# Performance work log

Hardware: AMD Instinct MI355X
Metric: run time of the kernel (lower is better)

Reference implementation:

```python
import jax, jax.numpy as jnp
import numpy as np

EPS = 1e-5
G, N, H, P, K = 8, 128, 64, 64, 4  # n_groups, d_state, n_heads, head_dim, conv kernel
R = H // G  # heads per group


def _rmsnorm(x, w, eps=EPS):
    return x * jax.lax.rsqrt(jnp.mean(x * x, axis=-1, keepdims=True) + eps) * w


def setup_inputs() -> dict:
    key = jax.random.key(0)
    ks = jax.random.split(key, 8)
    B, L, Dm = 2, 1024, 2048
    d_inner = 2 * Dm                      # 4096
    conv_dim = d_inner + 2 * G * N        # 6144
    proj_dim = 2 * d_inner + 2 * G * N + H  # 10304
    return {
        "hidden_states": jax.random.normal(ks[0], (B, L, Dm), jnp.float32),
        "residual": jax.random.normal(ks[1], (B, L, Dm), jnp.float32),
        "norm_w": jnp.ones((Dm,), jnp.float32),
        "in_proj_w": jax.random.normal(ks[2], (proj_dim, Dm), jnp.float32) * 0.02,
        "conv_w": jax.random.normal(ks[3], (conv_dim, K), jnp.float32) * 0.1,
        "conv_b": jnp.zeros((conv_dim,), jnp.float32),
        "A_log": jnp.log(jnp.arange(1, H + 1, dtype=jnp.float32)),
        "D_param": jnp.ones((H,), jnp.float32),
        "dt_bias": jax.random.uniform(ks[4], (H,), jnp.float32, -4.0, -1.0),
        "gate_norm_w": jnp.ones((d_inner,), jnp.float32),
        "out_proj_w": jax.random.normal(ks[5], (Dm, d_inner), jnp.float32) * 0.02,
    }


def reference(hidden_states, residual, norm_w, in_proj_w, conv_w, conv_b,
              A_log, D_param, dt_bias, gate_norm_w, out_proj_w):
    B, L, Dm = hidden_states.shape
    d_inner = 2 * Dm
    conv_dim = d_inner + 2 * G * N

    # fused residual-add RMSNorm (residual is not None branch)
    h = hidden_states + residual
    new_residual = h
    x = _rmsnorm(h, norm_w)

    # in_proj -> [z | xBC | dt]
    proj = jnp.einsum('bld,ed->ble', x, in_proj_w)
    z = proj[..., :d_inner]
    xBC = proj[..., d_inner:d_inner + conv_dim]
    dt = proj[..., d_inner + conv_dim:]            # [B, L, H]

    # causal depthwise conv1d over xBC, then SiLU
    lhs = jnp.transpose(xBC, (0, 2, 1))            # [B, C, L]
    rhs = conv_w[:, None, :]                       # [C, 1, K]
    conv = jax.lax.conv_general_dilated(
        lhs, rhs, window_strides=(1,), padding=[(K - 1, 0)],
        feature_group_count=conv_dim)
    xBC = jax.nn.silu(jnp.transpose(conv, (0, 2, 1)) + conv_b)

    xs = xBC[..., :d_inner].reshape(B, L, G, R, P)   # per-head inputs
    Bm = xBC[..., d_inner:d_inner + G * N].reshape(B, L, G, N)
    Cm = xBC[..., d_inner + G * N:].reshape(B, L, G, N)

    dt = jax.nn.softplus(dt + dt_bias)               # [B, L, H]
    A = -jnp.exp(A_log)                              # [H]
    dA = jnp.exp(dt * A).reshape(B, L, G, R)
    dtg = dt.reshape(B, L, G, R)

    # time-major for scan
    def step(hst, inp):
        dA_t, dt_t, x_t, B_t, C_t = inp            # [B,G,R], [B,G,R], [B,G,R,P], [B,G,N], [B,G,N]
        dBx = jnp.einsum('bgr,bgn,bgrp->bgrpn', dt_t, B_t, x_t)
        hst = hst * dA_t[..., None, None] + dBx    # [B,G,R,P,N]
        y_t = jnp.einsum('bgrpn,bgn->bgrp', hst, C_t)
        return hst, y_t

    tm = lambda a: jnp.moveaxis(a, 1, 0)
    h0 = jnp.zeros((B, G, R, P, N), hidden_states.dtype)
    _, ys = jax.lax.scan(step, h0, (tm(dA), tm(dtg), tm(xs), tm(Bm), tm(Cm)))
    y = jnp.moveaxis(ys, 0, 1)                     # [B, L, G, R, P]
    y = y + D_param.reshape(G, R)[None, None, :, :, None] * xs
    y = y.reshape(B, L, d_inner)

    # gated RMSNorm then out_proj
    y = _rmsnorm(y * jax.nn.silu(z), gate_norm_w)
    out = jnp.einsum('ble,de->bld', y, out_proj_w)
    return out, new_residual
```

## Files before the change

### kernel.cpp

```cpp
#include <hip/hip_runtime.h>

#define TOK 2048
#define DM 2048
#define DI 4096
#define NG 8
#define NN 128
#define PROJ_D 10304
#define PROJ_P 10496
#define CONV_D 6144
#define LSEQ 1024
#define CHUNK 64
#define NCHUNK 16

typedef unsigned short u16;
typedef __attribute__((ext_vector_type(4))) float f32x4;
typedef __attribute__((ext_vector_type(8))) short s16x8;
typedef __attribute__((ext_vector_type(4))) unsigned short u16x4;

__device__ __forceinline__ u16 f2bf(float f) {
  union { float f; unsigned u; } x; x.f = f;
  unsigned r = (x.u + 0x7FFFu + ((x.u >> 16) & 1u)) >> 16;
  return (u16)r;
}
__device__ __forceinline__ float bf2f(u16 u) {
  union { unsigned u; float f; } x; x.u = ((unsigned)u) << 16; return x.f;
}

__device__ __forceinline__ float blockReduceSum256(float s) {
  __shared__ float red[4];
  #pragma unroll
  for (int o = 32; o > 0; o >>= 1) s += __shfl_down(s, o, 64);
  int lane = threadIdx.x & 63, wid = threadIdx.x >> 6;
  if (lane == 0) red[wid] = s;
  __syncthreads();
  return red[0] + red[1] + red[2] + red[3];
}

__global__ __launch_bounds__(256) void cvt_bf16_pad(const float* __restrict__ src, u16* __restrict__ dst,
                                                    long n_src, long n_dst) {
  long i = ((long)blockIdx.x * 256 + threadIdx.x) * 4;
  if (i >= n_dst) return;
  u16x4 o;
  if (i < n_src) {
    f32x4 v = *(const f32x4*)&src[i];
    o.x = f2bf(v.x); o.y = f2bf(v.y); o.z = f2bf(v.z); o.w = f2bf(v.w);
  } else {
    o.x = 0; o.y = 0; o.z = 0; o.w = 0;
  }
  *(u16x4*)&dst[i] = o;
}

__global__ __launch_bounds__(256) void addnorm_kernel(const float* __restrict__ hs, const float* __restrict__ res,
        const float* __restrict__ w, float* __restrict__ nres, u16* __restrict__ xbf) {
  int row = blockIdx.x;
  size_t base = (size_t)row * DM;
  int tid = threadIdx.x;
  f32x4 h[2];
  float s = 0.f;
  #pragma unroll
  for (int i = 0; i < 2; i++) {
    int off = i * 1024 + tid * 4;
    f32x4 a = *(const f32x4*)&hs[base + off];
    f32x4 b = *(const f32x4*)&res[base + off];
    f32x4 v = a + b;
    h[i] = v;
    *(f32x4*)&nres[base + off] = v;
    s += v.x * v.x + v.y * v.y + v.z * v.z + v.w * v.w;
  }
  s = blockReduceSum256(s);
  float rs = rsqrtf(s * (1.f / DM) + 1e-5f);
  #pragma unroll
  for (int i = 0; i < 2; i++) {
    int off = i * 1024 + tid * 4;
    f32x4 wv = *(const f32x4*)&w[off];
    f32x4 v = h[i];
    u16x4 o;
    o.x = f2bf(v.x * rs * wv.x);
    o.y = f2bf(v.y * rs * wv.y);
    o.z = f2bf(v.z * rs * wv.z);
    o.w = f2bf(v.w * rs * wv.w);
    *(u16x4*)&xbf[base + off] = o;
  }
}

__device__ __forceinline__ void gld_lds16(const void* g, void* l) {
  __builtin_amdgcn_global_load_lds((const __attribute__((address_space(1))) void*)g,
                                   (__attribute__((address_space(3))) void*)l, 16, 0, 0);
}

template <bool BF16OUT>
__global__ __launch_bounds__(512, 2) void gemm8p(const u16* __restrict__ A, const u16* __restrict__ Bw,
                                                 void* __restrict__ Cv, int K, int Cstride, int nbx,
                                                 int nks, size_t part_stride) {
  __shared__ u16 As[2][256][64];
  __shared__ u16 Bs[2][256][64];
  int tid = threadIdx.x;
  int lane = tid & 63, w = tid >> 6;
  int wr = w >> 2, wc = w & 3;
  int cpx = gridDim.x >> 3;
  int bid = blockIdx.x;
  int lb = (bid & 7) * cpx + (bid >> 3);
  int ks = lb % nks;
  int tile = lb / nks;
  int by = tile / nbx, bx = tile - by * nbx;
  int Ks = K / nks;
  int k0 = ks * Ks;
  size_t m0 = (size_t)by * 256, n0 = (size_t)bx * 256;
  const u16* Ab = A + m0 * K;
  const u16* Bb = Bw + n0 * K;

  f32x4 acc[8][4];
  #pragma unroll
  for (int i = 0; i < 8; ++i)
    #pragma unroll
    for (int j = 0; j < 4; ++j) acc[i][j] = (f32x4){0.f, 0.f, 0.f, 0.f};

  int l3 = lane >> 3;
  int colsw = ((lane & 7) ^ l3) << 3;
  int fr = lane & 15, fq = lane >> 4;
  int pc0 = (fq * 8) ^ ((fr & 7) << 3);
  int pc1 = pc0 ^ 32;

  auto S = [&](int kt, int mat, int half) {
    int d = kt & 1;
    const u16* src = mat ? Bb : Ab;
    u16* dstbase = mat ? &Bs[d][0][0] : &As[d][0][0];
    #pragma unroll
    for (int j = 0; j < 2; ++j) {
      int rb = half * 128 + (w * 2 + j) * 8;
      gld_lds16(src + (size_t)(rb + l3) * K + k0 + kt * 64 + colsw, dstbase + rb * 64);
    }
  };

  int nkt = Ks >> 6;
  S(0, 1, 0); S(0, 1, 1); S(0, 0, 0); S(0, 0, 1);
  S(1, 1, 0); S(1, 1, 1);
  asm volatile("s_waitcnt vmcnt(4)" ::: "memory");
  __builtin_amdgcn_s_barrier();

  for (int kt = 0; kt < nkt; ++kt) {
    int d = kt & 1;
    s16x8 b[4][2];
    #pragma unroll
    for (int q = 0; q < 4; ++q) {
      if (q == 0) {
        #pragma unroll
        for (int ni = 0; ni < 4; ++ni) {
          b[ni][0] = *(const s16x8*)&Bs[d][wc * 64 + ni * 16 + fr][pc0];
          b[ni][1] = *(const s16x8*)&Bs[d][wc * 64 + ni * 16 + fr][pc1];
        }
      }
      s16x8 a[2][2];
      #pragma unroll
      for (int mi = 0; mi < 2; ++mi) {
        a[mi][0] = *(const s16x8*)&As[d][wr * 128 + q * 32 + mi * 16 + fr][pc0];
        a[mi][1] = *(const s16x8*)&As[d][wr * 128 + q * 32 + mi * 16 + fr][pc1];
      }
      if (q == 0)      { if (kt + 1 < nkt) S(kt + 1, 0, 0); }
      else if (q == 1) { if (kt + 1 < nkt) S(kt + 1, 0, 1); }
      else if (q == 2) { if (kt + 2 < nkt) S(kt + 2, 1, 0); }
      else {
        if (kt + 2 < nkt) { S(kt + 2, 1, 1); asm volatile("s_waitcnt vmcnt(4)" ::: "memory"); }
        else              { asm volatile("s_waitcnt vmcnt(0)" ::: "memory"); }
      }
      __builtin_amdgcn_s_barrier();
      __builtin_amdgcn_s_setprio(1);
      #pragma unroll
      for (int mi = 0; mi < 2; ++mi)
        #pragma unroll
        for (int ni = 0; ni < 4; ++ni) {
          acc[q * 2 + mi][ni] = __builtin_amdgcn_mfma_f32_16x16x32_bf16(a[mi][0], b[ni][0], acc[q * 2 + mi][ni], 0, 0, 0);
          acc[q * 2 + mi][ni] = __builtin_amdgcn_mfma_f32_16x16x32_bf16(a[mi][1], b[ni][1], acc[q * 2 + mi][ni], 0, 0, 0);
        }
      __builtin_amdgcn_s_setprio(0);
      __builtin_amdgcn_s_barrier();
    }
  }
  size_t crow0 = m0 + wr * 128 + fq * 4;
  size_t ccol0 = n0 + wc * 64 + fr;
  if constexpr (BF16OUT) {
    u16* C = (u16*)Cv;
    #pragma unroll
    for (int mf = 0; mf < 8; ++mf)
      #pragma unroll
      for (int ni = 0; ni < 4; ++ni)
        #pragma unroll
        for (int j = 0; j < 4; ++j)
          C[(crow0 + mf * 16 + j) * Cstride + ccol0 + ni * 16] = f2bf(acc[mf][ni][j]);
  } else {
    float* C = (float*)Cv + (size_t)ks * part_stride;
    #pragma unroll
    for (int mf = 0; mf < 8; ++mf)
      #pragma unroll
      for (int ni = 0; ni < 4; ++ni)
        #pragma unroll
        for (int j = 0; j < 4; ++j)
          C[(crow0 + mf * 16 + j) * Cstride + ccol0 + ni * 16] = acc[mf][ni][j];
  }
}

__global__ __launch_bounds__(256) void reduce4_kernel(const float* __restrict__ part, float* __restrict__ out) {
  size_t i = ((size_t)blockIdx.x * 256 + threadIdx.x) * 4;
  const size_t st = (size_t)TOK * DM;
  f32x4 s = *(const f32x4*)&part[i];
  s += *(const f32x4*)&part[i + st];
  s += *(const f32x4*)&part[i + 2 * st];
  s += *(const f32x4*)&part[i + 3 * st];
  *(f32x4*)&out[i] = s;
}

__global__ __launch_bounds__(256) void conv_silu_kernel(const u16* __restrict__ proj,
        const float* __restrict__ cw, const float* __restrict__ cb, u16* __restrict__ xbc) {
  long gid = (long)blockIdx.x * 256 + threadIdx.x;
  int c4 = (int)(gid % 1536);
  long t = gid / 1536;
  int l = (int)(t & 1023);
  int c = c4 * 4;
  const u16* base = proj + (size_t)t * PROJ_P + DI + c;
  f32x4 acc = *(const f32x4*)&cb[c];
  f32x4 w0 = *(const f32x4*)&cw[(c + 0) * 4];
  f32x4 w1 = *(const f32x4*)&cw[(c + 1) * 4];
  f32x4 w2 = *(const f32x4*)&cw[(c + 2) * 4];
  f32x4 w3 = *(const f32x4*)&cw[(c + 3) * 4];
  #pragma unroll
  for (int k = 0; k < 4; k++) {
    int ls = l - 3 + k;
    if (ls >= 0) {
      u16x4 v = *(const u16x4*)(base + ((long)(k - 3)) * PROJ_P);
      acc.x = fmaf(bf2f(v.x), w0[k], acc.x);
      acc.y = fmaf(bf2f(v.y), w1[k], acc.y);
      acc.z = fmaf(bf2f(v.z), w2[k], acc.z);
      acc.w = fmaf(bf2f(v.w), w3[k], acc.w);
    }
  }
  u16x4 o;
  o.x = f2bf(acc.x / (1.f + expf(-acc.x)));
  o.y = f2bf(acc.y / (1.f + expf(-acc.y)));
  o.z = f2bf(acc.z / (1.f + expf(-acc.z)));
  o.w = f2bf(acc.w / (1.f + expf(-acc.w)));
  *(u16x4*)&xbc[(size_t)t * CONV_D + c] = o;
}

__global__ __launch_bounds__(256) void dt_kernel(const u16* __restrict__ proj, const float* __restrict__ dt_bias,
        const float* __restrict__ A_log, float* __restrict__ dtspT, float* __restrict__ dtaT) {
  int idx = blockIdx.x * 256 + threadIdx.x;
  int t = idx >> 6, hh = idx & 63;
  int b = t >> 10, l = t & 1023;
  float dtv = bf2f(proj[(size_t)t * PROJ_P + (DI + CONV_D) + hh]) + dt_bias[hh];
  float sp = (dtv > 15.f) ? dtv : log1pf(expf(dtv));
  float Ah = -expf(A_log[hh]);
  size_t o = (size_t)(b * 64 + hh) * LSEQ + l;
  dtspT[o] = sp;
  dtaT[o] = sp * Ah;
}

__global__ __launch_bounds__(512) void ssd_kernel(const u16* __restrict__ xbc, const float* __restrict__ dtsp,
        const float* __restrict__ dta, const float* __restrict__ Dp, u16* __restrict__ y) {
  int bid = blockIdx.x;
  int g = bid & 7, b = (bid >> 3) & 1, r = (bid >> 4) & 7, ph = bid >> 7;
  int h = g * 8 + r;
  int p0 = ph * 32;
  int tid = threadIdx.x;
  int w = tid >> 6, lane = tid & 63;

  __shared__ u16 Bsh[2][64][128];
  __shared__ u16 Csh[2][64][128];
  __shared__ u16 Xt[2][32][64];
  __shared__ u16 Btw[2][128][64];
  __shared__ u16 GWsh[64][64];
  __shared__ u16 Hbf[32][128];
  __shared__ float dtsh[LSEQ];
  __shared__ float Lsh[LSEQ];

  const float* dtrow = dtsp + (size_t)(b * 64 + h) * LSEQ;
  const float* dtarow = dta + (size_t)(b * 64 + h) * LSEQ;
  if (tid < 256) { f32x4 v = *(const f32x4*)&dtrow[tid * 4]; *(f32x4*)&dtsh[tid * 4] = v; }
  for (int cc = w; cc < NCHUNK; cc += 8) {
    float a = dtarow[cc * 64 + lane];
    #pragma unroll
    for (int o = 1; o < 64; o <<= 1) { float t2 = __shfl_up(a, o, 64); if (lane >= o) a += t2; }
    Lsh[cc * 64 + lane] = a;
  }
  {
    u16* hp = &Hbf[0][0];
    for (int i = tid; i < 1024; i += 512) *(u16x4*)&hp[i * 4] = (u16x4){0, 0, 0, 0};
  }
  float Dv = Dp[h];
  const u16* xb = xbc + (size_t)b * LSEQ * CONV_D;
  int swz = (lane & 7) << 3;
  __syncthreads();

  auto stage = [&](int cc, int d) {
    int t0c = cc * 64;
    int pw = w - 4, ptid = tid - 256;
    #pragma unroll
    for (int q = 0; q < 4; ++q) {
      int rowb = pw * 16 + q * 4;
      int row = rowb + (lane >> 4);
      int colb = ((lane & 15) * 8) ^ ((row & 7) << 3);
      gld_lds16(xb + (size_t)(t0c + row) * CONV_D + DI + g * 128 + colb, &Bsh[d][rowb][0]);
      gld_lds16(xb + (size_t)(t0c + row) * CONV_D + DI + NG * NN + g * 128 + colb, &Csh[d][rowb][0]);
    }
    {
      int s = ptid & 63, pq = ptid >> 6;
      const u16* xr = xb + (size_t)(t0c + s) * CONV_D + g * 512 + r * 64 + p0;
      #pragma unroll
      for (int pb = 0; pb < 2; ++pb) {
        int pl0 = pb * 16 + pq * 4;
        u16x4 v = *(const u16x4*)&xr[pl0];
        #pragma unroll
        for (int j = 0; j < 4; ++j) {
          int p = pl0 + j;
          Xt[d][p][s ^ ((p & 7) << 3)] = v[j];
        }
      }
    }
    {
      int s = ptid & 63, nq = ptid >> 6;
      float wend = __expf(Lsh[t0c + 63] - Lsh[t0c + s]) * dtsh[t0c + s];
      const u16* br = xb + (size_t)(t0c + s) * CONV_D + DI + g * 128;
      #pragma unroll
      for (int nb = 0; nb < 8; ++nb) {
        int n0 = nb * 16 + nq * 4;
        u16x4 v = *(const u16x4*)&br[n0];
        #pragma unroll
        for (int j = 0; j < 4; ++j) {
          int n = n0 + j;
          Btw[d][n][s ^ ((n & 7) << 3)] = f2bf(bf2f(v[j]) * wend);
        }
      }
    }
  };

  if (w >= 4) stage(0, 0);
  __syncthreads();

  f32x4 hst[2][2];
  #pragma unroll
  for (int i = 0; i < 2; ++i)
    #pragma unroll
    for (int j = 0; j < 2; ++j) hst[i][j] = (f32x4){0.f, 0.f, 0.f, 0.f};

  for (int c = 0; c < NCHUNK; ++c) {
    int d = c & 1;
    int t0c = c * 64;
    if (w >= 4) {
      if (c + 1 < NCHUNK) stage(c + 1, d ^ 1);
    } else {
      s16x8 aC[4];
      #pragma unroll
      for (int k = 0; k < 4; ++k)
        aC[k] = *(const s16x8*)&Csh[d][w * 16 + (lane & 15)][(k * 32 + (lane >> 4) * 8) ^ swz];
      f32x4 Gacc[4];
      #pragma unroll
      for (int st = 0; st < 4; ++st) Gacc[st] = (f32x4){0.f, 0.f, 0.f, 0.f};
      #pragma unroll
      for (int st = 0; st < 4; ++st)
        #pragma unroll
        for (int k = 0; k < 4; ++k) {
          s16x8 bB = *(const s16x8*)&Bsh[d][st * 16 + (lane & 15)][(k * 32 + (lane >> 4) * 8) ^ swz];
          Gacc[st] = __builtin_amdgcn_mfma_f32_16x16x32_bf16(aC[k], bB, Gacc[st], 0, 0, 0);
        }
      #pragma unroll
      for (int st = 0; st < 4; ++st) {
        int s = st * 16 + (lane & 15);
        float Ls = Lsh[t0c + s], dts = dtsh[t0c + s];
        #pragma unroll
        for (int j = 0; j < 4; ++j) {
          int t = w * 16 + (lane >> 4) * 4 + j;
          float wgt = (s <= t) ? __expf(Lsh[t0c + t] - Ls) * dts : 0.f;
          GWsh[t][s ^ ((t & 7) << 3)] = f2bf(Gacc[st][j] * wgt);
        }
      }
      f32x4 Yacc[2], Y2acc[2];
      #pragma unroll
      for (int pt = 0; pt < 2; ++pt) { Yacc[pt] = (f32x4){0.f,0.f,0.f,0.f}; Y2acc[pt] = (f32x4){0.f,0.f,0.f,0.f}; }
      s16x8 aGW[2];
      #pragma unroll
      for (int k = 0; k < 2; ++k)
        aGW[k] = *(const s16x8*)&GWsh[w * 16 + (lane & 15)][(k * 32 + (lane >> 4) * 8) ^ swz];
      #pragma unroll
      for (int pt = 0; pt < 2; ++pt) {
        #pragma unroll
        for (int k = 0; k < 2; ++k) {
          s16x8 bX = *(const s16x8*)&Xt[d][pt * 16 + (lane & 15)][(k * 32 + (lane >> 4) * 8) ^ swz];
          Yacc[pt] = __builtin_amdgcn_mfma_f32_16x16x32_bf16(aGW[k], bX, Yacc[pt], 0, 0, 0);
        }
        #pragma unroll
        for (int k = 0; k < 4; ++k) {
          s16x8 bH = *(const s16x8*)&Hbf[pt * 16 + (lane & 15)][(k * 32 + (lane >> 4) * 8) ^ swz];
          Y2acc[pt] = __builtin_amdgcn_mfma_f32_16x16x32_bf16(aC[k], bH, Y2acc[pt], 0, 0, 0);
        }
      }
      float el[4];
      #pragma unroll
      for (int j = 0; j < 4; ++j) el[j] = __expf(Lsh[t0c + w * 16 + (lane >> 4) * 4 + j]);
      #pragma unroll
      for (int pt = 0; pt < 2; ++pt) {
        int p = pt * 16 + (lane & 15);
        #pragma unroll
        for (int j = 0; j < 4; ++j) {
          int t = w * 16 + (lane >> 4) * 4 + j;
          float xv = bf2f(Xt[d][p][t ^ ((p & 7) << 3)]);
          float yv = Yacc[pt][j] + el[j] * Y2acc[pt][j] + Dv * xv;
          y[((size_t)b * LSEQ + t0c + t) * DI + g * 512 + r * 64 + p0 + p] = f2bf(yv);
        }
      }
      float e63 = __expf(Lsh[t0c + 63]);
      s16x8 aX[2][2];
      #pragma unroll
      for (int mp = 0; mp < 2; ++mp)
        #pragma unroll
        for (int k = 0; k < 2; ++k)
          aX[mp][k] = *(const s16x8*)&Xt[d][mp * 16 + (lane & 15)][(k * 32 + (lane >> 4) * 8) ^ swz];
      #pragma unroll
      for (int mp = 0; mp < 2; ++mp)
        #pragma unroll
        for (int nn = 0; nn < 2; ++nn) {
          #pragma unroll
          for (int j = 0; j < 4; ++j) hst[mp][nn][j] *= e63;
          #pragma unroll
          for (int k = 0; k < 2; ++k) {
            s16x8 bW = *(const s16x8*)&Btw[d][w * 32 + nn * 16 + (lane & 15)][(k * 32 + (lane >> 4) * 8) ^ swz];
            hst[mp][nn] = __builtin_amdgcn_mfma_f32_16x16x32_bf16(aX[mp][k], bW, hst[mp][nn], 0, 0, 0);
          }
        }
    }
    __syncthreads();
    if (w < 4) {
      #pragma unroll
      for (int mp = 0; mp < 2; ++mp)
        #pragma unroll
        for (int nn = 0; nn < 2; ++nn) {
          int n = w * 32 + nn * 16 + (lane & 15);
          #pragma unroll
          for (int j = 0; j < 4; ++j) {
            int p = mp * 16 + (lane >> 4) * 4 + j;
            Hbf[p][n ^ ((p & 7) << 3)] = f2bf(hst[mp][nn][j]);
          }
        }
    }
    __syncthreads();
  }
}

__global__ __launch_bounds__(256) void gate_kernel(const u16* __restrict__ y, const u16* __restrict__ proj,
        const float* __restrict__ gw, u16* __restrict__ y2) {
  int row = blockIdx.x;
  const u16* yr = y + (size_t)row * DI;
  const u16* zr = proj + (size_t)row * PROJ_P;
  int tid = threadIdx.x;
  f32x4 v[4];
  float s = 0.f;
  #pragma unroll
  for (int i = 0; i < 4; i++) {
    int off = i * 1024 + tid * 4;
    u16x4 av = *(const u16x4*)&yr[off];
    u16x4 zv = *(const u16x4*)&zr[off];
    f32x4 t;
    float z0 = bf2f(zv.x), z1 = bf2f(zv.y), z2 = bf2f(zv.z), z3 = bf2f(zv.w);
    t.x = bf2f(av.x) * (z0 / (1.f + expf(-z0)));
    t.y = bf2f(av.y) * (z1 / (1.f + expf(-z1)));
    t.z = bf2f(av.z) * (z2 / (1.f + expf(-z2)));
    t.w = bf2f(av.w) * (z3 / (1.f + expf(-z3)));
    v[i] = t;
    s += t.x * t.x + t.y * t.y + t.z * t.z + t.w * t.w;
  }
  s = blockReduceSum256(s);
  float rs = rsqrtf(s * (1.f / DI) + 1e-5f);
  #pragma unroll
  for (int i = 0; i < 4; i++) {
    int off = i * 1024 + tid * 4;
    f32x4 wv = *(const f32x4*)&gw[off];
    u16x4 o;
    o.x = f2bf(v[i].x * rs * wv.x);
    o.y = f2bf(v[i].y * rs * wv.y);
    o.z = f2bf(v[i].z * rs * wv.z);
    o.w = f2bf(v[i].w * rs * wv.w);
    *(u16x4*)&y2[(size_t)row * DI + off] = o;
  }
}

extern "C" void kernel_launch(void* const* d_in, const int* in_sizes, int n_in,
                              void* d_out, int out_size, void* d_ws, size_t ws_size,
                              hipStream_t stream) {
  (void)in_sizes; (void)n_in; (void)out_size; (void)ws_size;
  const float* hs      = (const float*)d_in[0];
  const float* res     = (const float*)d_in[1];
  const float* norm_w  = (const float*)d_in[2];
  const float* w_in    = (const float*)d_in[3];
  const float* conv_w  = (const float*)d_in[4];
  const float* conv_b  = (const float*)d_in[5];
  const float* A_log   = (const float*)d_in[6];
  const float* D_param = (const float*)d_in[7];
  const float* dt_bias = (const float*)d_in[8];
  const float* gate_w  = (const float*)d_in[9];
  const float* w_out   = (const float*)d_in[10];

  float* out  = (float*)d_out;
  float* nres = out + (size_t)TOK * DM;

  char* ws = (char*)d_ws;
  size_t off = 0;
  u16*   WB1  = (u16*)(ws + off);   off += (size_t)PROJ_P * DM * 2;
  u16*   WB2  = (u16*)(ws + off);   off += (size_t)DM * DI * 2;
  u16*   XBF  = (u16*)(ws + off);   off += (size_t)TOK * DM * 2;
  u16*   PROJ = (u16*)(ws + off);   off += (size_t)TOK * PROJ_P * 2;
  u16*   XBC  = (u16*)(ws + off);   off += (size_t)TOK * CONV_D * 2;
  float* DTSP = (float*)(ws + off); off += (size_t)TOK * 64 * 4;
  float* DTA  = (float*)(ws + off); off += (size_t)TOK * 64 * 4;
  u16*   Y    = (u16*)(ws + off);   off += (size_t)TOK * DI * 2;
  u16*   Y2   = (u16*)(ws + off);   off += (size_t)TOK * DI * 2;
  float* PART = (float*)(ws + off); off += (size_t)4 * TOK * DM * 4;

  cvt_bf16_pad<<<20992, 256, 0, stream>>>(w_in, WB1, (long)PROJ_D * DM, (long)PROJ_P * DM);
  cvt_bf16_pad<<<8192, 256, 0, stream>>>(w_out, WB2, (long)DM * DI, (long)DM * DI);
  addnorm_kernel<<<TOK, 256, 0, stream>>>(hs, res, norm_w, nres, XBF);
  gemm8p<true><<<(TOK / 256) * (PROJ_P / 256), 512, 0, stream>>>(XBF, WB1, PROJ, DM, PROJ_P, PROJ_P / 256, 1, 0);
  conv_silu_kernel<<<(TOK * (CONV_D / 4)) / 256, 256, 0, stream>>>(PROJ, conv_w, conv_b, XBC);
  dt_kernel<<<(TOK * 64) / 256, 256, 0, stream>>>(PROJ, dt_bias, A_log, DTSP, DTA);
  ssd_kernel<<<256, 512, 0, stream>>>(XBC, DTSP, DTA, D_param, Y);
  gate_kernel<<<TOK, 256, 0, stream>>>(Y, PROJ, gate_w, Y2);
  gemm8p<false><<<(TOK / 256) * (DM / 256) * 4, 512, 0, stream>>>(Y2, WB2, PART, DI, DM, DM / 256, 4, (size_t)TOK * DM);
  reduce4_kernel<<<(TOK * DM) / 1024, 256, 0, stream>>>(PART, out);
}
```

Baseline: 305.6 us.

## Use smaller-tile triple-buffered GEMM for in_proj

Adds a new GEMM kernel with 128x256 output tiles, a K-step of 32, triple-buffered LDS loads via global_load_lds, and an XOR swizzle, then uses it for the in_proj matmul. Smaller tiles double the number of blocks (656 vs 328) to fill the GPU better, and the lower LDS use allows 4 blocks per CU. The trade-off is less operand reuse per tile and more barriers per unit of work.

```diff
diff --git a/kernel.cpp b/kernel.cpp
--- a/kernel.cpp
+++ b/kernel.cpp
@@ -86,6 +86,103 @@
 __device__ __forceinline__ void gld_lds16(const void* g, void* l) {
   __builtin_amdgcn_global_load_lds((const __attribute__((address_space(1))) void*)g,
                                    (__attribute__((address_space(3))) void*)l, 16, 0, 0);
+}
+
+template <bool BF16OUT>
+__global__ __launch_bounds__(512, 4) void gemm32(const u16* __restrict__ A, const u16* __restrict__ Bw,
+                                                 void* __restrict__ Cv, int K, int Cstride, int nbx) {
+  __shared__ u16 As[3][128][32];
+  __shared__ u16 Bs[3][256][32];
+  int tid = threadIdx.x;
+  int lane = tid & 63, w = tid >> 6;
+  int wr = w >> 2, wc = w & 3;
+  int cpx = gridDim.x >> 3;
+  int bid = blockIdx.x;
+  int lb = (bid & 7) * cpx + (bid >> 3);
+  int by = lb / nbx, bx = lb - by * nbx;
+  size_t m0 = (size_t)by * 128, n0 = (size_t)bx * 256;
+  const u16* Ab = A + m0 * K;
+  const u16* Bb = Bw + n0 * K;
+
+  f32x4 acc[4][4];
+  #pragma unroll
+  for (int i = 0; i < 4; ++i)
+    #pragma unroll
+    for (int j = 0; j < 4; ++j) acc[i][j] = (f32x4){0.f, 0.f, 0.f, 0.f};
+
+  int fr = lane & 15, fq = lane >> 4;
+  int lrow = lane >> 2, lg = lane & 3;
+
+  auto S = [&](int kt) {
+    int bu = kt % 3;
+    {
+      int row = w * 16 + lrow;
+      int cs = (lg ^ ((row >> 1) & 3)) * 8;
+      gld_lds16(Ab + (size_t)row * K + kt * 32 + cs, &As[bu][w * 16][0]);
+    }
+    #pragma unroll
+    for (int j = 0; j < 2; ++j) {
+      int row = j * 128 + w * 16 + lrow;
+      int cs = (lg ^ ((row >> 1) & 3)) * 8;
+      gld_lds16(Bb + (size_t)row * K + kt * 32 + cs, &Bs[bu][j * 128 + w * 16][0]);
+    }
+  };
+
+  int nkt = K >> 5;
+  S(0); S(1);
+  asm volatile("s_waitcnt vmcnt(3)" ::: "memory");
+  __builtin_amdgcn_s_barrier();
+
+  for (int kt = 0; kt < nkt; ++kt) {
+    int bu = kt % 3;
+    s16x8 a[4], b[4];
+    #pragma unroll
+    for (int mi = 0; mi < 4; ++mi) {
+      int row = wr * 64 + mi * 16 + fr;
+      a[mi] = *(const s16x8*)&As[bu][row][(fq ^ ((row >> 1) & 3)) * 8];
+    }
+    #pragma unroll
+    for (int ni = 0; ni < 4; ++ni) {
+      int row = wc * 64 + ni * 16 + fr;
+      b[ni] = *(const s16x8*)&Bs[bu][row][(fq ^ ((row >> 1) & 3)) * 8];
+    }
+    if (kt + 2 < nkt) {
+      S(kt + 2);
+      asm volatile("s_waitcnt vmcnt(3)" ::: "memory");
+    } else {
+      asm volatile("s_waitcnt vmcnt(0)" ::: "memory");
+    }
+    __builtin_amdgcn_s_barrier();
+    __builtin_amdgcn_s_setprio(1);
+    #pragma unroll
+    for (int mi = 0; mi < 4; ++mi)
+      #pragma unroll
+      for (int ni = 0; ni < 4; ++ni)
+        acc[mi][ni] = __builtin_amdgcn_mfma_f32_16x16x32_bf16(a[mi], b[ni], acc[mi][ni], 0, 0, 0);
+    __builtin_amdgcn_s_setprio(0);
+    __builtin_amdgcn_s_barrier();
+  }
+  size_t crow0 = m0 + wr * 64 + fq * 4;
+  size_t ccol0 = n0 + wc * 64 + fr;
+  if constexpr (BF16OUT) {
+    u16* C = (u16*)Cv;
+    #pragma unroll
+    for (int mi = 0; mi < 4; ++mi)
+      #pragma unroll
+      for (int ni = 0; ni < 4; ++ni)
+        #pragma unroll
+        for (int j = 0; j < 4; ++j)
+          C[(crow0 + mi * 16 + j) * Cstride + ccol0 + ni * 16] = f2bf(acc[mi][ni][j]);
+  } else {
+    float* C = (float*)Cv;
+    #pragma unroll
+    for (int mi = 0; mi < 4; ++mi)
+      #pragma unroll
+      for (int ni = 0; ni < 4; ++ni)
+        #pragma unroll
+        for (int j = 0; j < 4; ++j)
+          C[(crow0 + mi * 16 + j) * Cstride + ccol0 + ni * 16] = acc[mi][ni][j];
+  }
 }
 
 template <bool BF16OUT>
@@ -516,7 +613,7 @@
   cvt_bf16_pad<<<20992, 256, 0, stream>>>(w_in, WB1, (long)PROJ_D * DM, (long)PROJ_P * DM);
   cvt_bf16_pad<<<8192, 256, 0, stream>>>(w_out, WB2, (long)DM * DI, (long)DM * DI);
   addnorm_kernel<<<TOK, 256, 0, stream>>>(hs, res, norm_w, nres, XBF);
-  gemm8p<true><<<(TOK / 256) * (PROJ_P / 256), 512, 0, stream>>>(XBF, WB1, PROJ, DM, PROJ_P, PROJ_P / 256, 1, 0);
+  gemm32<true><<<(TOK / 128) * (PROJ_P / 256), 512, 0, stream>>>(XBF, WB1, PROJ, DM, PROJ_P, PROJ_P / 256);
   conv_silu_kernel<<<(TOK * (CONV_D / 4)) / 256, 256, 0, stream>>>(PROJ, conv_w, conv_b, XBC);
   dt_kernel<<<(TOK * 64) / 256, 256, 0, stream>>>(PROJ, dt_bias, A_log, DTSP, DTA);
   ssd_kernel<<<256, 512, 0, stream>>>(XBC, DTSP, DTA, D_param, Y);
```

Measured after the change: 308.0 us. Within noise of the previous version (+0.8%).
